# Performance work log

Measured on AMD Instinct MI355X. Metric: run time of the kernel, lower is better.

The kernel has to match this reference:

```python
import jax, jax.numpy as jnp
import numpy as np

D = 1024
H = 16
HD = D // H
SCALE = HD ** -0.5
EPS = 1e-5

def _ln(x, g, b):
    m = jnp.mean(x, axis=-1, keepdims=True)
    v = jnp.mean((x - m) ** 2, axis=-1, keepdims=True)
    return (x - m) / jnp.sqrt(v + EPS) * g + b

def setup_inputs() -> dict:
    key = jax.random.key(0)
    ks = jax.random.split(key, 16)
    B, Lq, Lk = 8, 1024, 1024
    s = 0.02
    inp = {
        "q": jax.random.normal(ks[0], (B, Lq, D), jnp.float32),
        "kv": jax.random.normal(ks[1], (B, Lk, D), jnp.float32),
        "kv_mask": jax.random.randint(ks[2], (B, Lk), 0, 2).astype(bool),
        "Wq": jax.random.normal(ks[3], (D, D), jnp.float32) * s,
        "bq": jnp.zeros((D,), jnp.float32),
        "Wk": jax.random.normal(ks[4], (D, D), jnp.float32) * s,
        "bk": jnp.zeros((D,), jnp.float32),
        "Wv": jax.random.normal(ks[5], (D, D), jnp.float32) * s,
        "bv": jnp.zeros((D,), jnp.float32),
        "Wo": jax.random.normal(ks[6], (D, D), jnp.float32) * s,
        "bo": jnp.zeros((D,), jnp.float32),
        "ln1_g": jnp.ones((D,), jnp.float32),
        "ln1_b": jnp.zeros((D,), jnp.float32),
        "W1": jax.random.normal(ks[7], (D, 4 * D), jnp.float32) * s,
        "b1": jnp.zeros((4 * D,), jnp.float32),
        "W2": jax.random.normal(ks[8], (4 * D, D), jnp.float32) * s,
        "b2": jnp.zeros((D,), jnp.float32),
        "ln2_g": jnp.ones((D,), jnp.float32),
        "ln2_b": jnp.zeros((D,), jnp.float32),
    }
    return inp

def reference(q, kv, kv_mask, Wq, bq, Wk, bk, Wv, bv, Wo, bo, ln1_g, ln1_b, W1, b1, W2, b2, ln2_g, ln2_b):
    B, Lq, _ = q.shape
    Lk = kv.shape[1]
    # projections -> [B, H, L, HD]
    qp = (q @ Wq + bq).reshape(B, Lq, H, HD).transpose(0, 2, 1, 3)
    kp = (kv @ Wk + bk).reshape(B, Lk, H, HD).transpose(0, 2, 1, 3)
    vp = (kv @ Wv + bv).reshape(B, Lk, H, HD).transpose(0, 2, 1, 3)
    scores = jnp.einsum('bhqd,bhkd->bhqk', qp, kp) * SCALE
    # mask: True = pad; if a row is all-pad, un-mask the last key position
    all_pad = jnp.all(kv_mask, axis=1)  # [B]
    mask = kv_mask.at[:, -1].set(jnp.where(all_pad, False, kv_mask[:, -1]))
    scores = jnp.where(mask[:, None, None, :], jnp.float32(-10000.0), scores)
    attn = jax.nn.softmax(scores, axis=-1)  # dropout is identity at eval
    out = jnp.einsum('bhqk,bhkd->bhqd', attn, vp)
    out = out.transpose(0, 2, 1, 3).reshape(B, Lq, D)
    out = out @ Wo + bo
    x = _ln(q + out, ln1_g, ln1_b)
    x2 = jax.nn.relu(x @ W1 + b1) @ W2 + b2
    return _ln(x + x2, ln2_g, ln2_b)
```

## Files before the change

kernel.cpp:

```cpp
#include <hip/hip_runtime.h>

typedef __bf16 bf16_t;
typedef bf16_t bf16x8 __attribute__((ext_vector_type(8)));
typedef bf16_t bf16x4 __attribute__((ext_vector_type(4)));
typedef float f32x4 __attribute__((ext_vector_type(4)));
typedef unsigned int u32;

typedef __attribute__((address_space(1))) unsigned as1_u32;
typedef __attribute__((address_space(3))) unsigned as3_u32;

#define LOG2E 1.4426950408889634f
#define QSCALE (0.125f * LOG2E)
#define MASK2 (-10000.0f * LOG2E)

__device__ __forceinline__ void gload16(const void* g, void* l) {
  __builtin_amdgcn_global_load_lds((as1_u32*)(void*)g, (as3_u32*)l, 16, 0, 0);
}

__global__ void cvt_qkv(const float* __restrict__ q, const float* __restrict__ kv,
                        bf16_t* __restrict__ qb, bf16_t* __restrict__ kvb) {
  long i = ((long)blockIdx.x * 256 + threadIdx.x) * 8;
  const float* src; bf16_t* dst;
  if (i < 8388608) { src = q + i; dst = qb + i; }
  else { src = kv + (i - 8388608); dst = kvb + (i - 8388608); }
  const float4 a = *(const float4*)src;
  const float4 b = *(const float4*)(src + 4);
  bf16x8 o;
  o[0] = (bf16_t)a.x; o[1] = (bf16_t)a.y; o[2] = (bf16_t)a.z; o[3] = (bf16_t)a.w;
  o[4] = (bf16_t)b.x; o[5] = (bf16_t)b.y; o[6] = (bf16_t)b.z; o[7] = (bf16_t)b.w;
  *(bf16x8*)dst = o;
}

__global__ void prep_mask(const unsigned char* __restrict__ mraw,
                          float* __restrict__ maskf) {
  __shared__ int sred[256];
  const int t = threadIdx.x, b = blockIdx.x;
  int f = 0;
  for (int i = t; i < 2048; i += 256) {
    u32 v = ((const u32*)mraw)[i];
    if (v & 0xFFFFFF00u) f = 1;
  }
  sred[t] = f; __syncthreads();
  for (int s = 128; s; s >>= 1) { if (t < s) sred[t] |= sred[t + s]; __syncthreads(); }
  const int isByte = sred[0];
  __syncthreads();

  int vals[4]; int allpad = 1;
#pragma unroll
  for (int i = 0; i < 4; i++) {
    int k = t * 4 + i;
    int mv = isByte ? (int)mraw[b * 1024 + k] : ((const int*)mraw)[b * 1024 + k];
    vals[i] = (mv != 0);
    allpad &= vals[i];
  }
  sred[t] = allpad; __syncthreads();
  for (int s = 128; s; s >>= 1) { if (t < s) sred[t] &= sred[t + s]; __syncthreads(); }
  const int ap = sred[0];
#pragma unroll
  for (int i = 0; i < 4; i++) {
    int k = t * 4 + i;
    int m = vals[i];
    if (ap && k == 1023) m = 0;
    maskf[b * 1024 + k] = m ? MASK2 : 0.0f;
  }
}

struct TP { const float* s; bf16_t* d; int K; int N; };
struct TP6 { TP t[6]; };
__global__ void transpose_all(TP6 args) {
  __shared__ float tile[64][65];
  int bid = blockIdx.x, z, tx, ty;
  if (bid < 1024)      { z = bid >> 8;  int r = bid & 255;  tx = r & 15; ty = r >> 4; }
  else if (bid < 2048) { z = 4;         int r = bid - 1024; tx = r & 63; ty = r >> 6; }
  else                 { z = 5;         int r = bid - 2048; tx = r & 15; ty = r >> 4; }
  const TP a = args.t[z];
  const int t = threadIdx.x;
  const int n0 = tx * 64, k0 = ty * 64;
#pragma unroll
  for (int i = 0; i < 16; i++) {
    int e = i * 256 + t; int r = e >> 6, c = e & 63;
    tile[r][c] = a.s[(size_t)(k0 + r) * a.N + n0 + c];
  }
  __syncthreads();
#pragma unroll
  for (int i = 0; i < 16; i++) {
    int e = i * 256 + t; int r = e >> 6, c = e & 63;
    a.d[(size_t)(n0 + r) * a.K + k0 + c] = (bf16_t)tile[c][r];
  }
}

template<int BM, int BN, int NT>
__global__ __launch_bounds__(NT, 2)
void gemm_bt(const bf16_t* __restrict__ A, const bf16_t* __restrict__ BT,
             const float* __restrict__ bias, bf16_t* __restrict__ C,
             int M, int N, int K, int relu, int bias_mode, float scale) {
  constexpr int WAVES = NT / 64;
  constexpr int WNC = (BN == 256) ? 4 : 2;
  constexpr int WMC = WAVES / WNC;
  constexpr int M_REP = BM / (WMC * 16);
  constexpr int N_REP = BN / (WNC * 16);
  constexpr int JA = BM * 8 / NT;
  constexpr int JB = BN * 8 / NT;

  __shared__ __align__(16) bf16_t As[2][BM * 64];
  __shared__ __align__(16) bf16_t Bs[2][BN * 64];

  const int tid = threadIdx.x;
  const int wave = tid >> 6, lane = tid & 63;
  const int quad = lane >> 4, l15 = lane & 15;
  const int gx = gridDim.x;
  const int nwg = gx * gridDim.y;
  int lin = blockIdx.y * gx + blockIdx.x;
  lin = (lin & 7) * (nwg >> 3) + (lin >> 3);
  const long bm = (long)(lin / gx) * BM, bn = (long)(lin % gx) * BN;
  const int wm = (wave / WNC) * (M_REP * 16), wn = (wave % WNC) * (N_REP * 16);

  const bf16_t* agp[JA];
  const bf16_t* bgp[JB];
#pragma unroll
  for (int j = 0; j < JA; j++) {
    int e = j * NT + tid, r = e >> 3, c = (e & 7) ^ (r & 7);
    agp[j] = A + (bm + r) * (long)K + c * 8;
  }
#pragma unroll
  for (int j = 0; j < JB; j++) {
    int e = j * NT + tid, r = e >> 3, c = (e & 7) ^ (r & 7);
    bgp[j] = BT + (bn + r) * (long)K + c * 8;
  }

  int aoff[M_REP][2], boff[N_REP][2];
#pragma unroll
  for (int mi = 0; mi < M_REP; mi++)
#pragma unroll
    for (int ks = 0; ks < 2; ks++) {
      int row = wm + mi * 16 + l15;
      aoff[mi][ks] = row * 64 + (((ks * 4 + quad) ^ (row & 7)) * 8);
    }
#pragma unroll
  for (int ni = 0; ni < N_REP; ni++)
#pragma unroll
    for (int ks = 0; ks < 2; ks++) {
      int row = wn + ni * 16 + l15;
      boff[ni][ks] = row * 64 + (((ks * 4 + quad) ^ (row & 7)) * 8);
    }

  f32x4 acc[M_REP][N_REP];
#pragma unroll
  for (int i = 0; i < M_REP; i++)
#pragma unroll
    for (int j = 0; j < N_REP; j++) acc[i][j] = (f32x4){0.f, 0.f, 0.f, 0.f};

  auto stage = [&](int kt, int s) {
#pragma unroll
    for (int j = 0; j < JA; j++)
      gload16(agp[j] + (long)kt * 64, &As[s][(j * NT + wave * 64) * 8]);
#pragma unroll
    for (int j = 0; j < JB; j++)
      gload16(bgp[j] + (long)kt * 64, &Bs[s][(j * NT + wave * 64) * 8]);
  };

  const int T = K >> 6;
  stage(0, 0);
  for (int t = 0; t < T; t++) {
    const int s = t & 1;
    if (t + 1 < T) {
      stage(t + 1, s ^ 1);
      asm volatile("s_waitcnt vmcnt(8)" ::: "memory");
    } else {
      asm volatile("s_waitcnt vmcnt(0)" ::: "memory");
    }
    __builtin_amdgcn_s_barrier();

#pragma unroll
    for (int ks = 0; ks < 2; ks++) {
      bf16x8 af[M_REP], bf[N_REP];
#pragma unroll
      for (int mi = 0; mi < M_REP; mi++) af[mi] = *(const bf16x8*)&As[s][aoff[mi][ks]];
#pragma unroll
      for (int ni = 0; ni < N_REP; ni++) bf[ni] = *(const bf16x8*)&Bs[s][boff[ni][ks]];
      __builtin_amdgcn_s_setprio(1);
#pragma unroll
      for (int mi = 0; mi < M_REP; mi++)
#pragma unroll
        for (int ni = 0; ni < N_REP; ni++)
          acc[mi][ni] = __builtin_amdgcn_mfma_f32_16x16x32_bf16(af[mi], bf[ni], acc[mi][ni], 0, 0, 0);
      __builtin_amdgcn_s_setprio(0);
    }
    asm volatile("s_waitcnt lgkmcnt(0)" ::: "memory");
    __builtin_amdgcn_s_barrier();
  }

#pragma unroll
  for (int mi = 0; mi < M_REP; mi++) {
#pragma unroll
    for (int ni = 0; ni < N_REP; ni++) {
      const long col = bn + wn + ni * 16 + l15;
      const float bc = bias_mode ? 0.f : bias[col];
#pragma unroll
      for (int r = 0; r < 4; r++) {
        const long row = bm + wm + mi * 16 + quad * 4 + r;
        const float bb = bias_mode ? bias[row] : bc;
        float v = (acc[mi][ni][r] + bb) * scale;
        if (relu) v = v > 0.f ? v : 0.f;
        C[row * N + col] = (bf16_t)v;
      }
    }
  }
}

__global__ __launch_bounds__(512, 2)
void gemm_8p(const bf16_t* __restrict__ A, const bf16_t* __restrict__ BT,
             const float* __restrict__ bias, bf16_t* __restrict__ C,
             int M, int N, int K, int relu, float scale) {
  __shared__ __align__(16) bf16_t As[2][256 * 64];
  __shared__ __align__(16) bf16_t Bs[2][256 * 64];

  const int tid = threadIdx.x;
  const int wave = tid >> 6, lane = tid & 63;
  const int quad = lane >> 4, l15 = lane & 15;
  const int g = wave >> 2;
  const int wn = (wave & 3) * 64;
  const int gx = gridDim.x;
  const int nwg = gx * gridDim.y;
  int lin = blockIdx.y * gx + blockIdx.x;
  lin = (lin & 7) * (nwg >> 3) + (lin >> 3);
  const long bm = (long)(lin / gx) * 256, bn = (long)(lin % gx) * 256;

  const int r_ = tid >> 3;
  const int cs_ = ((tid & 7) ^ (r_ & 7)) * 8;
  const int arow = r_ + ((r_ >= 32) ? 96 : 0);
  const bf16_t* ag = A + (bm + arow) * (long)K + cs_;
  const bf16_t* bg = BT + (bn + r_) * (long)K + cs_;

  int aoff[4][2][2], boff[4][2];
#pragma unroll
  for (int p = 0; p < 4; p++)
#pragma unroll
    for (int i = 0; i < 2; i++)
#pragma unroll
      for (int ks = 0; ks < 2; ks++) {
        int slot = p * 64 + g * 32 + i * 16 + l15;
        aoff[p][i][ks] = slot * 64 + (((ks * 4 + quad) ^ (l15 & 7)) * 8);
      }
#pragma unroll
  for (int ni = 0; ni < 4; ni++)
#pragma unroll
    for (int ks = 0; ks < 2; ks++) {
      int row = wn + ni * 16 + l15;
      boff[ni][ks] = row * 64 + (((ks * 4 + quad) ^ (row & 7)) * 8);
    }

  f32x4 acc[8][4];
#pragma unroll
  for (int i = 0; i < 8; i++)
#pragma unroll
    for (int j = 0; j < 4; j++) acc[i][j] = (f32x4){0.f, 0.f, 0.f, 0.f};

  auto stageB = [&](int kt, int s, int j) {
    gload16(bg + (long)(j * 64) * K + (long)kt * 64, &Bs[s][(j * 512 + wave * 64) * 8]);
  };
  auto stageA = [&](int kt, int s, int p) {
    gload16(ag + (long)(p * 32) * K + (long)kt * 64, &As[s][(p * 512 + wave * 64) * 8]);
  };

  const int T = K >> 6;
#pragma unroll
  for (int j = 0; j < 4; j++) stageB(0, 0, j);
#pragma unroll
  for (int p = 0; p < 4; p++) stageA(0, 0, p);

#pragma unroll 1
  for (int t = 0; t < T; t++) {
    const int s = t & 1;
    const bool pf = (t + 1 < T);

    bf16x8 bf[4][2];
#pragma unroll
    for (int p = 0; p < 4; p++) {
      if (p == 0)      { asm volatile("s_waitcnt vmcnt(3)" ::: "memory"); }
      else if (p == 1) { if (pf) asm volatile("s_waitcnt vmcnt(4)" ::: "memory");
                         else    asm volatile("s_waitcnt vmcnt(2)" ::: "memory"); }
      else if (p == 2) { if (pf) asm volatile("s_waitcnt vmcnt(5)" ::: "memory");
                         else    asm volatile("s_waitcnt vmcnt(1)" ::: "memory"); }
      else             { if (pf) asm volatile("s_waitcnt vmcnt(6)" ::: "memory");
                         else    asm volatile("s_waitcnt vmcnt(0)" ::: "memory"); }
      __builtin_amdgcn_s_barrier();

      if (p == 0) {
#pragma unroll
        for (int ni = 0; ni < 4; ni++)
#pragma unroll
          for (int ks = 0; ks < 2; ks++)
            bf[ni][ks] = *(const bf16x8*)&Bs[s][boff[ni][ks]];
      }
      bf16x8 af[2][2];
#pragma unroll
      for (int i = 0; i < 2; i++)
#pragma unroll
        for (int ks = 0; ks < 2; ks++)
          af[i][ks] = *(const bf16x8*)&As[s][aoff[p][i][ks]];

      if (pf) {
        if (p == 0)      { stageB(t + 1, s ^ 1, 0); stageB(t + 1, s ^ 1, 1); }
        else if (p == 1) { stageB(t + 1, s ^ 1, 2); stageB(t + 1, s ^ 1, 3); }
        else if (p == 2) { stageA(t + 1, s ^ 1, 0); stageA(t + 1, s ^ 1, 1); }
        else             { stageA(t + 1, s ^ 1, 2); stageA(t + 1, s ^ 1, 3); }
      }

      __builtin_amdgcn_s_setprio(1);
#pragma unroll
      for (int i = 0; i < 2; i++)
#pragma unroll
        for (int ni = 0; ni < 4; ni++)
#pragma unroll
          for (int ks = 0; ks < 2; ks++)
            acc[p * 2 + i][ni] = __builtin_amdgcn_mfma_f32_16x16x32_bf16(
                af[i][ks], bf[ni][ks], acc[p * 2 + i][ni], 0, 0, 0);
      __builtin_amdgcn_s_setprio(0);
    }
  }

#pragma unroll
  for (int mi = 0; mi < 8; mi++) {
#pragma unroll
    for (int ni = 0; ni < 4; ni++) {
      const long col = bn + wn + ni * 16 + l15;
      const float bc = bias[col];
#pragma unroll
      for (int r = 0; r < 4; r++) {
        const long row = bm + g * 128 + mi * 16 + quad * 4 + r;
        float v = (acc[mi][ni][r] + bc) * scale;
        if (relu) v = v > 0.f ? v : 0.f;
        C[row * N + col] = (bf16_t)v;
      }
    }
  }
}

__global__ __launch_bounds__(256, 4)
void attn(const bf16_t* __restrict__ Q, const bf16_t* __restrict__ Kp,
          const bf16_t* __restrict__ Vt, const float* __restrict__ maskf,
          bf16_t* __restrict__ AO) {
  __shared__ __align__(16) bf16_t Qs[64 * 64];
  __shared__ __align__(16) bf16_t Ks[64 * 64];
  __shared__ __align__(16) bf16_t Vts[64 * 64];
  __shared__ __align__(16) bf16_t Ps[4][16 * 64];
  __shared__ __align__(16) float msk[64];

  const int tid = threadIdx.x;
  const int wave = tid >> 6, lane = tid & 63;
  const int quad = lane >> 4, l15 = lane & 15;
  int lin = (blockIdx.z * 16 + blockIdx.y) * 16 + blockIdx.x;
  lin = (lin & 7) * 256 + (lin >> 3);
  const int q0 = (lin & 15) * 64;
  const int h = (lin >> 4) & 15;
  const int b = lin >> 8;

  const long base_q = ((long)b * 1024 + q0) * 1024 + h * 64;
  const long base_k = (long)b * 1024 * 1024 + h * 64;
  const long base_v = (long)h * 64 * 8192 + b * 1024;

  const int r0 = tid >> 3;
  const int c0 = ((tid & 7) ^ (r0 & 7)) * 8;
  const int r1 = (256 + tid) >> 3;
  const int c1 = (((256 + tid) & 7) ^ (r1 & 7)) * 8;
  const int wd0 = wave * 64 * 8;
  const int wd1 = (256 + wave * 64) * 8;

  const bf16_t* qg0 = Q + base_q + (long)r0 * 1024 + c0;
  const bf16_t* qg1 = Q + base_q + (long)r1 * 1024 + c1;
  const bf16_t* kg0 = Kp + base_k + (long)r0 * 1024 + c0;
  const bf16_t* kg1 = Kp + base_k + (long)r1 * 1024 + c1;
  const bf16_t* vg0 = Vt + base_v + (long)r0 * 8192 + c0;
  const bf16_t* vg1 = Vt + base_v + (long)r1 * 8192 + c1;
  const float* mrow = maskf + b * 1024;

  gload16(qg0, &Qs[wd0]);
  gload16(qg1, &Qs[wd1]);

  int offKV[4][2], offP[2], pwOff[4];
#pragma unroll
  for (int nt = 0; nt < 4; nt++)
#pragma unroll
    for (int ks = 0; ks < 2; ks++)
      offKV[nt][ks] = (nt * 16 + l15) * 64 + (((ks * 4 + quad) ^ (l15 & 7)) * 8);
#pragma unroll
  for (int ks = 0; ks < 2; ks++)
    offP[ks] = l15 * 64 + (((ks * 4 + quad) ^ (l15 & 7)) * 8);
#pragma unroll
  for (int nt = 0; nt < 4; nt++)
    pwOff[nt] = l15 * 64 + (((nt * 2 + (quad >> 1)) ^ (l15 & 7)) * 8) + (quad & 1) * 4;

  __syncthreads();

  bf16x8 aq[2];
#pragma unroll
  for (int ks = 0; ks < 2; ks++) {
    const int row = wave * 16 + l15;
    aq[ks] = *(const bf16x8*)&Qs[row * 64 + (((ks * 4 + quad) ^ (row & 7)) * 8)];
  }

  float l_i = 0.f;
  f32x4 o[4];
#pragma unroll
  for (int nt = 0; nt < 4; nt++) o[nt] = (f32x4){0.f, 0.f, 0.f, 0.f};

  bf16_t* Pw = &Ps[wave][0];

  for (int kt = 0; kt < 16; kt++) {
    const int k0 = kt * 64;
    __syncthreads();
    gload16(kg0 + (long)k0 * 1024, &Ks[wd0]);
    gload16(kg1 + (long)k0 * 1024, &Ks[wd1]);
    gload16(vg0 + k0, &Vts[wd0]);
    gload16(vg1 + k0, &Vts[wd1]);
    if (tid < 64) msk[tid] = mrow[k0 + tid];
    __syncthreads();

    f32x4 mv[4];
#pragma unroll
    for (int nt = 0; nt < 4; nt++)
      mv[nt] = *(const f32x4*)&msk[nt * 16 + quad * 4];

    f32x4 sc[4];
#pragma unroll
    for (int nt = 0; nt < 4; nt++) {
      f32x4 s = mv[nt];
#pragma unroll
      for (int ks = 0; ks < 2; ks++) {
        bf16x8 bk = *(const bf16x8*)&Ks[offKV[nt][ks]];
        s = __builtin_amdgcn_mfma_f32_16x16x32_bf16(bk, aq[ks], s, 0, 0, 0);
      }
      sc[nt] = s;
    }

#pragma unroll
    for (int nt = 0; nt < 4; nt++)
#pragma unroll
      for (int r = 0; r < 4; r++) {
        const float p = exp2f(sc[nt][r]);
        sc[nt][r] = p;
        l_i += p;
      }

#pragma unroll
    for (int nt = 0; nt < 4; nt++) {
      bf16x4 pv;
#pragma unroll
      for (int r = 0; r < 4; r++) pv[r] = (bf16_t)sc[nt][r];
      *(bf16x4*)&Pw[pwOff[nt]] = pv;
    }

#pragma unroll
    for (int ks = 0; ks < 2; ks++) {
      bf16x8 ap = *(const bf16x8*)&Pw[offP[ks]];
#pragma unroll
      for (int nt = 0; nt < 4; nt++) {
        bf16x8 bv = *(const bf16x8*)&Vts[offKV[nt][ks]];
        o[nt] = __builtin_amdgcn_mfma_f32_16x16x32_bf16(ap, bv, o[nt], 0, 0, 0);
      }
    }
  }

  l_i += __shfl_xor(l_i, 16);
  l_i += __shfl_xor(l_i, 32);
  float linv[4];
#pragma unroll
  for (int r = 0; r < 4; r++)
    linv[r] = 1.0f / __shfl(l_i, (quad << 4) | (quad * 4 + r));
#pragma unroll
  for (int r = 0; r < 4; r++) {
    const int row = q0 + wave * 16 + quad * 4 + r;
#pragma unroll
    for (int nt = 0; nt < 4; nt++) {
      const int col = h * 64 + nt * 16 + l15;
      AO[((long)b * 1024 + row) * 1024 + col] = (bf16_t)(o[nt][r] * linv[r]);
    }
  }
}

__global__ __launch_bounds__(256)
void ln_res1(const float* __restrict__ xa, const bf16_t* __restrict__ xb,
             const float* __restrict__ g, const float* __restrict__ bt,
             bf16_t* __restrict__ out) {
  __shared__ float sw[8];
  const int t = threadIdx.x, w = t >> 6;
  const long row = blockIdx.x;
  const float4 a = *(const float4*)(xa + row * 1024 + t * 4);
  const bf16x4 bq = *(const bf16x4*)(xb + row * 1024 + t * 4);
  float v[4] = {a.x + (float)bq[0], a.y + (float)bq[1],
                a.z + (float)bq[2], a.w + (float)bq[3]};
  float s = v[0] + v[1] + v[2] + v[3];
  float s2 = v[0]*v[0] + v[1]*v[1] + v[2]*v[2] + v[3]*v[3];
#pragma unroll
  for (int off = 1; off < 64; off <<= 1) {
    s += __shfl_xor(s, off); s2 += __shfl_xor(s2, off);
  }
  if ((t & 63) == 0) { sw[w] = s; sw[4 + w] = s2; }
  __syncthreads();
  s = sw[0] + sw[1] + sw[2] + sw[3];
  s2 = sw[4] + sw[5] + sw[6] + sw[7];
  const float mean = s * (1.f / 1024.f);
  const float var = s2 * (1.f / 1024.f) - mean * mean;
  const float rstd = rsqrtf(var + 1e-5f);
  bf16x4 o;
#pragma unroll
  for (int i = 0; i < 4; i++) {
    const int c = t * 4 + i;
    o[i] = (bf16_t)((v[i] - mean) * rstd * g[c] + bt[c]);
  }
  *(bf16x4*)(out + row * 1024 + t * 4) = o;
}

__global__ __launch_bounds__(256)
void ln_res2(const bf16_t* __restrict__ xa, const bf16_t* __restrict__ xb,
             const float* __restrict__ g, const float* __restrict__ bt,
             float* __restrict__ out) {
  __shared__ float sw[8];
  const int t = threadIdx.x, w = t >> 6;
  const long row = blockIdx.x;
  const bf16x4 aq = *(const bf16x4*)(xa + row * 1024 + t * 4);
  const bf16x4 bq = *(const bf16x4*)(xb + row * 1024 + t * 4);
  float v[4];
#pragma unroll
  for (int i = 0; i < 4; i++) v[i] = (float)aq[i] + (float)bq[i];
  float s = v[0] + v[1] + v[2] + v[3];
  float s2 = v[0]*v[0] + v[1]*v[1] + v[2]*v[2] + v[3]*v[3];
#pragma unroll
  for (int off = 1; off < 64; off <<= 1) {
    s += __shfl_xor(s, off); s2 += __shfl_xor(s2, off);
  }
  if ((t & 63) == 0) { sw[w] = s; sw[4 + w] = s2; }
  __syncthreads();
  s = sw[0] + sw[1] + sw[2] + sw[3];
  s2 = sw[4] + sw[5] + sw[6] + sw[7];
  const float mean = s * (1.f / 1024.f);
  const float var = s2 * (1.f / 1024.f) - mean * mean;
  const float rstd = rsqrtf(var + 1e-5f);
  float4 o;
  o.x = (v[0] - mean) * rstd * g[t*4+0] + bt[t*4+0];
  o.y = (v[1] - mean) * rstd * g[t*4+1] + bt[t*4+1];
  o.z = (v[2] - mean) * rstd * g[t*4+2] + bt[t*4+2];
  o.w = (v[3] - mean) * rstd * g[t*4+3] + bt[t*4+3];
  *(float4*)(out + row * 1024 + t * 4) = o;
}

extern "C" void kernel_launch(void* const* d_in, const int* in_sizes, int n_in,
                              void* d_out, int out_size, void* d_ws, size_t ws_size,
                              hipStream_t stream) {
  (void)in_sizes; (void)n_in; (void)out_size; (void)ws_size;
  const float* q   = (const float*)d_in[0];
  const float* kv  = (const float*)d_in[1];
  const unsigned char* mraw = (const unsigned char*)d_in[2];
  const float* Wq = (const float*)d_in[3];
  const float* bq = (const float*)d_in[4];
  const float* Wk = (const float*)d_in[5];
  const float* bk = (const float*)d_in[6];
  const float* Wv = (const float*)d_in[7];
  const float* bv = (const float*)d_in[8];
  const float* Wo = (const float*)d_in[9];
  const float* bo = (const float*)d_in[10];
  const float* g1 = (const float*)d_in[11];
  const float* be1 = (const float*)d_in[12];
  const float* W1 = (const float*)d_in[13];
  const float* b1 = (const float*)d_in[14];
  const float* W2 = (const float*)d_in[15];
  const float* b2 = (const float*)d_in[16];
  const float* g2 = (const float*)d_in[17];
  const float* be2 = (const float*)d_in[18];
  float* out = (float*)d_out;

  char* ws = (char*)d_ws;
  size_t off = 0;
  auto alloc = [&](size_t bytes) -> char* {
    char* p = ws + off; off += (bytes + 255) & ~(size_t)255; return p;
  };
  const size_t MB16 = (size_t)8192 * 1024 * 2;
  float*  maskf = (float*)alloc(8192 * 4);
  bf16_t* WqT = (bf16_t*)alloc((size_t)1024 * 1024 * 2);
  bf16_t* WkT = (bf16_t*)alloc((size_t)1024 * 1024 * 2);
  bf16_t* WvT = (bf16_t*)alloc((size_t)1024 * 1024 * 2);
  bf16_t* WoT = (bf16_t*)alloc((size_t)1024 * 1024 * 2);
  bf16_t* W1T = (bf16_t*)alloc((size_t)1024 * 4096 * 2);
  bf16_t* W2T = (bf16_t*)alloc((size_t)4096 * 1024 * 2);
  bf16_t* Qp = (bf16_t*)alloc(MB16);
  bf16_t* Kp = (bf16_t*)alloc(MB16);
  bf16_t* VT = (bf16_t*)alloc(MB16);
  bf16_t* AO = (bf16_t*)alloc(MB16);
  bf16_t* X1 = (bf16_t*)alloc(MB16);
  bf16_t* TL = (bf16_t*)alloc(MB16);
  bf16_t* qb  = X1;
  bf16_t* kvb = TL;
  bf16_t* HF  = Qp;
  bf16_t* OP  = Kp;
  bf16_t* F2  = WqT;

  cvt_qkv<<<8192, 256, 0, stream>>>(q, kv, qb, kvb);
  prep_mask<<<8, 256, 0, stream>>>(mraw, maskf);
  TP6 tp = {{ {Wq, WqT, 1024, 1024}, {Wk, WkT, 1024, 1024},
              {Wv, WvT, 1024, 1024}, {Wo, WoT, 1024, 1024},
              {W1, W1T, 1024, 4096}, {W2, W2T, 4096, 1024} }};
  transpose_all<<<3072, 256, 0, stream>>>(tp);

  const dim3 gproj(8, 64);
  gemm_bt<128,128,256><<<gproj, 256, 0, stream>>>(qb,  WqT, bq, Qp, 8192, 1024, 1024, 0, 0, QSCALE);
  gemm_bt<128,128,256><<<gproj, 256, 0, stream>>>(kvb, WkT, bk, Kp, 8192, 1024, 1024, 0, 0, 1.f);
  gemm_bt<128,128,256><<<dim3(64, 8), 256, 0, stream>>>(WvT, kvb, bv, VT, 1024, 8192, 1024, 0, 1, 1.f);

  attn<<<dim3(16, 16, 8), 256, 0, stream>>>(Qp, Kp, VT, maskf, AO);

  gemm_bt<128,128,256><<<gproj, 256, 0, stream>>>(AO, WoT, bo, OP, 8192, 1024, 1024, 0, 0, 1.f);
  ln_res1<<<8192, 256, 0, stream>>>(q, OP, g1, be1, X1);

  gemm_8p<<<dim3(16, 32), 512, 0, stream>>>(X1, W1T, b1, HF, 8192, 4096, 1024, 1, 1.f);
  gemm_bt<128,128,256><<<gproj, 256, 0, stream>>>(HF, W2T, b2, F2, 8192, 1024, 4096, 0, 0, 1.f);
  ln_res2<<<8192, 256, 0, stream>>>(X1, F2, g2, be2, out);
}
```

Baseline: 514.0 us.

## Replace 128x128 GEMMs with templated 8-wave 256xBN phased-pipeline GEMM

Removes the simple double-buffered 128x128 gemm_bt kernel and generalizes the 8-wave, 4-phase interleaved-prefetch gemm_8p kernel over BN (128 or 256), adding bias_mode support. All projection, output and FFN2 GEMMs now use 256x128 tiles with 512 threads, and prefetch is spread across phases with adjusted vmcnt waits. The intent is more reuse per tile and better overlap of loads with MFMA. In exchange there are fewer workgroups (256 per GEMM) on a many-CU device, and the handwritten wait counts are more fragile.

```diff
diff --git a/kernel.cpp b/kernel.cpp
--- a/kernel.cpp
+++ b/kernel.cpp
@@ -89,142 +89,26 @@
   }
 }
 
-template<int BM, int BN, int NT>
-__global__ __launch_bounds__(NT, 2)
-void gemm_bt(const bf16_t* __restrict__ A, const bf16_t* __restrict__ BT,
+template<int BN>
+__global__ __launch_bounds__(512, 2)
+void gemm_8p(const bf16_t* __restrict__ A, const bf16_t* __restrict__ BT,
              const float* __restrict__ bias, bf16_t* __restrict__ C,
              int M, int N, int K, int relu, int bias_mode, float scale) {
-  constexpr int WAVES = NT / 64;
-  constexpr int WNC = (BN == 256) ? 4 : 2;
-  constexpr int WMC = WAVES / WNC;
-  constexpr int M_REP = BM / (WMC * 16);
-  constexpr int N_REP = BN / (WNC * 16);
-  constexpr int JA = BM * 8 / NT;
-  constexpr int JB = BN * 8 / NT;
-
-  __shared__ __align__(16) bf16_t As[2][BM * 64];
+  constexpr int JB = BN * 8 / 512;
+  constexpr int N_REP = BN / 64;
+  __shared__ __align__(16) bf16_t As[2][256 * 64];
   __shared__ __align__(16) bf16_t Bs[2][BN * 64];
 
   const int tid = threadIdx.x;
   const int wave = tid >> 6, lane = tid & 63;
   const int quad = lane >> 4, l15 = lane & 15;
+  const int g = wave >> 2;
+  const int wn = (wave & 3) * (N_REP * 16);
   const int gx = gridDim.x;
   const int nwg = gx * gridDim.y;
   int lin = blockIdx.y * gx + blockIdx.x;
   lin = (lin & 7) * (nwg >> 3) + (lin >> 3);
-  const long bm = (long)(lin / gx) * BM, bn = (long)(lin % gx) * BN;
-  const int wm = (wave / WNC) * (M_REP * 16), wn = (wave % WNC) * (N_REP * 16);
-
-  const bf16_t* agp[JA];
-  const bf16_t* bgp[JB];
-#pragma unroll
-  for (int j = 0; j < JA; j++) {
-    int e = j * NT + tid, r = e >> 3, c = (e & 7) ^ (r & 7);
-    agp[j] = A + (bm + r) * (long)K + c * 8;
-  }
-#pragma unroll
-  for (int j = 0; j < JB; j++) {
-    int e = j * NT + tid, r = e >> 3, c = (e & 7) ^ (r & 7);
-    bgp[j] = BT + (bn + r) * (long)K + c * 8;
-  }
-
-  int aoff[M_REP][2], boff[N_REP][2];
-#pragma unroll
-  for (int mi = 0; mi < M_REP; mi++)
-#pragma unroll
-    for (int ks = 0; ks < 2; ks++) {
-      int row = wm + mi * 16 + l15;
-      aoff[mi][ks] = row * 64 + (((ks * 4 + quad) ^ (row & 7)) * 8);
-    }
-#pragma unroll
-  for (int ni = 0; ni < N_REP; ni++)
-#pragma unroll
-    for (int ks = 0; ks < 2; ks++) {
-      int row = wn + ni * 16 + l15;
-      boff[ni][ks] = row * 64 + (((ks * 4 + quad) ^ (row & 7)) * 8);
-    }
-
-  f32x4 acc[M_REP][N_REP];
-#pragma unroll
-  for (int i = 0; i < M_REP; i++)
-#pragma unroll
-    for (int j = 0; j < N_REP; j++) acc[i][j] = (f32x4){0.f, 0.f, 0.f, 0.f};
-
-  auto stage = [&](int kt, int s) {
-#pragma unroll
-    for (int j = 0; j < JA; j++)
-      gload16(agp[j] + (long)kt * 64, &As[s][(j * NT + wave * 64) * 8]);
-#pragma unroll
-    for (int j = 0; j < JB; j++)
-      gload16(bgp[j] + (long)kt * 64, &Bs[s][(j * NT + wave * 64) * 8]);
-  };
-
-  const int T = K >> 6;
-  stage(0, 0);
-  for (int t = 0; t < T; t++) {
-    const int s = t & 1;
-    if (t + 1 < T) {
-      stage(t + 1, s ^ 1);
-      asm volatile("s_waitcnt vmcnt(8)" ::: "memory");
-    } else {
-      asm volatile("s_waitcnt vmcnt(0)" ::: "memory");
-    }
-    __builtin_amdgcn_s_barrier();
-
-#pragma unroll
-    for (int ks = 0; ks < 2; ks++) {
-      bf16x8 af[M_REP], bf[N_REP];
-#pragma unroll
-      for (int mi = 0; mi < M_REP; mi++) af[mi] = *(const bf16x8*)&As[s][aoff[mi][ks]];
-#pragma unroll
-      for (int ni = 0; ni < N_REP; ni++) bf[ni] = *(const bf16x8*)&Bs[s][boff[ni][ks]];
-      __builtin_amdgcn_s_setprio(1);
-#pragma unroll
-      for (int mi = 0; mi < M_REP; mi++)
-#pragma unroll
-        for (int ni = 0; ni < N_REP; ni++)
-          acc[mi][ni] = __builtin_amdgcn_mfma_f32_16x16x32_bf16(af[mi], bf[ni], acc[mi][ni], 0, 0, 0);
-      __builtin_amdgcn_s_setprio(0);
-    }
-    asm volatile("s_waitcnt lgkmcnt(0)" ::: "memory");
-    __builtin_amdgcn_s_barrier();
-  }
-
-#pragma unroll
-  for (int mi = 0; mi < M_REP; mi++) {
-#pragma unroll
-    for (int ni = 0; ni < N_REP; ni++) {
-      const long col = bn + wn + ni * 16 + l15;
-      const float bc = bias_mode ? 0.f : bias[col];
-#pragma unroll
-      for (int r = 0; r < 4; r++) {
-        const long row = bm + wm + mi * 16 + quad * 4 + r;
-        const float bb = bias_mode ? bias[row] : bc;
-        float v = (acc[mi][ni][r] + bb) * scale;
-        if (relu) v = v > 0.f ? v : 0.f;
-        C[row * N + col] = (bf16_t)v;
-      }
-    }
-  }
-}
-
-__global__ __launch_bounds__(512, 2)
-void gemm_8p(const bf16_t* __restrict__ A, const bf16_t* __restrict__ BT,
-             const float* __restrict__ bias, bf16_t* __restrict__ C,
-             int M, int N, int K, int relu, float scale) {
-  __shared__ __align__(16) bf16_t As[2][256 * 64];
-  __shared__ __align__(16) bf16_t Bs[2][256 * 64];
-
-  const int tid = threadIdx.x;
-  const int wave = tid >> 6, lane = tid & 63;
-  const int quad = lane >> 4, l15 = lane & 15;
-  const int g = wave >> 2;
-  const int wn = (wave & 3) * 64;
-  const int gx = gridDim.x;
-  const int nwg = gx * gridDim.y;
-  int lin = blockIdx.y * gx + blockIdx.x;
-  lin = (lin & 7) * (nwg >> 3) + (lin >> 3);
-  const long bm = (long)(lin / gx) * 256, bn = (long)(lin % gx) * 256;
+  const long bm = (long)(lin / gx) * 256, bn = (long)(lin % gx) * BN;
 
   const int r_ = tid >> 3;
   const int cs_ = ((tid & 7) ^ (r_ & 7)) * 8;
@@ -232,7 +116,7 @@
   const bf16_t* ag = A + (bm + arow) * (long)K + cs_;
   const bf16_t* bg = BT + (bn + r_) * (long)K + cs_;
 
-  int aoff[4][2][2], boff[4][2];
+  int aoff[4][2][2], boff[N_REP][2];
 #pragma unroll
   for (int p = 0; p < 4; p++)
 #pragma unroll
@@ -243,18 +127,18 @@
         aoff[p][i][ks] = slot * 64 + (((ks * 4 + quad) ^ (l15 & 7)) * 8);
       }
 #pragma unroll
-  for (int ni = 0; ni < 4; ni++)
+  for (int ni = 0; ni < N_REP; ni++)
 #pragma unroll
     for (int ks = 0; ks < 2; ks++) {
       int row = wn + ni * 16 + l15;
       boff[ni][ks] = row * 64 + (((ks * 4 + quad) ^ (row & 7)) * 8);
     }
 
-  f32x4 acc[8][4];
+  f32x4 acc[8][N_REP];
 #pragma unroll
   for (int i = 0; i < 8; i++)
 #pragma unroll
-    for (int j = 0; j < 4; j++) acc[i][j] = (f32x4){0.f, 0.f, 0.f, 0.f};
+    for (int j = 0; j < N_REP; j++) acc[i][j] = (f32x4){0.f, 0.f, 0.f, 0.f};
 
   auto stageB = [&](int kt, int s, int j) {
     gload16(bg + (long)(j * 64) * K + (long)kt * 64, &Bs[s][(j * 512 + wave * 64) * 8]);
@@ -265,7 +149,7 @@
 
   const int T = K >> 6;
 #pragma unroll
-  for (int j = 0; j < 4; j++) stageB(0, 0, j);
+  for (int j = 0; j < JB; j++) stageB(0, 0, j);
 #pragma unroll
   for (int p = 0; p < 4; p++) stageA(0, 0, p);
 
@@ -274,21 +158,31 @@
     const int s = t & 1;
     const bool pf = (t + 1 < T);
 
-    bf16x8 bf[4][2];
+    bf16x8 bf[N_REP][2];
 #pragma unroll
     for (int p = 0; p < 4; p++) {
-      if (p == 0)      { asm volatile("s_waitcnt vmcnt(3)" ::: "memory"); }
-      else if (p == 1) { if (pf) asm volatile("s_waitcnt vmcnt(4)" ::: "memory");
-                         else    asm volatile("s_waitcnt vmcnt(2)" ::: "memory"); }
-      else if (p == 2) { if (pf) asm volatile("s_waitcnt vmcnt(5)" ::: "memory");
-                         else    asm volatile("s_waitcnt vmcnt(1)" ::: "memory"); }
-      else             { if (pf) asm volatile("s_waitcnt vmcnt(6)" ::: "memory");
-                         else    asm volatile("s_waitcnt vmcnt(0)" ::: "memory"); }
+      if constexpr (JB == 4) {
+        if (p == 0)      { asm volatile("s_waitcnt vmcnt(3)" ::: "memory"); }
+        else if (p == 1) { if (pf) asm volatile("s_waitcnt vmcnt(4)" ::: "memory");
+                           else    asm volatile("s_waitcnt vmcnt(2)" ::: "memory"); }
+        else if (p == 2) { if (pf) asm volatile("s_waitcnt vmcnt(5)" ::: "memory");
+                           else    asm volatile("s_waitcnt vmcnt(1)" ::: "memory"); }
+        else             { if (pf) asm volatile("s_waitcnt vmcnt(6)" ::: "memory");
+                           else    asm volatile("s_waitcnt vmcnt(0)" ::: "memory"); }
+      } else {
+        if (p == 0)      { asm volatile("s_waitcnt vmcnt(3)" ::: "memory"); }
+        else if (p == 1) { if (pf) asm volatile("s_waitcnt vmcnt(3)" ::: "memory");
+                           else    asm volatile("s_waitcnt vmcnt(2)" ::: "memory"); }
+        else if (p == 2) { if (pf) asm volatile("s_waitcnt vmcnt(3)" ::: "memory");
+                           else    asm volatile("s_waitcnt vmcnt(1)" ::: "memory"); }
+        else             { if (pf) asm volatile("s_waitcnt vmcnt(4)" ::: "memory");
+                           else    asm volatile("s_waitcnt vmcnt(0)" ::: "memory"); }
+      }
       __builtin_amdgcn_s_barrier();
 
       if (p == 0) {
 #pragma unroll
-        for (int ni = 0; ni < 4; ni++)
+        for (int ni = 0; ni < N_REP; ni++)
 #pragma unroll
           for (int ks = 0; ks < 2; ks++)
             bf[ni][ks] = *(const bf16x8*)&Bs[s][boff[ni][ks]];
@@ -301,17 +195,24 @@
           af[i][ks] = *(const bf16x8*)&As[s][aoff[p][i][ks]];
 
       if (pf) {
-        if (p == 0)      { stageB(t + 1, s ^ 1, 0); stageB(t + 1, s ^ 1, 1); }
-        else if (p == 1) { stageB(t + 1, s ^ 1, 2); stageB(t + 1, s ^ 1, 3); }
-        else if (p == 2) { stageA(t + 1, s ^ 1, 0); stageA(t + 1, s ^ 1, 1); }
-        else             { stageA(t + 1, s ^ 1, 2); stageA(t + 1, s ^ 1, 3); }
+        if constexpr (JB == 4) {
+          if (p == 0)      { stageB(t + 1, s ^ 1, 0); stageB(t + 1, s ^ 1, 1); }
+          else if (p == 1) { stageB(t + 1, s ^ 1, 2); stageB(t + 1, s ^ 1, 3); }
+          else if (p == 2) { stageA(t + 1, s ^ 1, 0); stageA(t + 1, s ^ 1, 1); }
+          else             { stageA(t + 1, s ^ 1, 2); stageA(t + 1, s ^ 1, 3); }
+        } else {
+          if (p == 0)      { stageB(t + 1, s ^ 1, 0); }
+          else if (p == 1) { stageB(t + 1, s ^ 1, 1); }
+          else if (p == 2) { stageA(t + 1, s ^ 1, 0); stageA(t + 1, s ^ 1, 1); }
+          else             { stageA(t + 1, s ^ 1, 2); stageA(t + 1, s ^ 1, 3); }
+        }
       }
 
       __builtin_amdgcn_s_setprio(1);
 #pragma unroll
       for (int i = 0; i < 2; i++)
 #pragma unroll
-        for (int ni = 0; ni < 4; ni++)
+        for (int ni = 0; ni < N_REP; ni++)
 #pragma unroll
           for (int ks = 0; ks < 2; ks++)
             acc[p * 2 + i][ni] = __builtin_amdgcn_mfma_f32_16x16x32_bf16(
@@ -323,13 +224,14 @@
 #pragma unroll
   for (int mi = 0; mi < 8; mi++) {
 #pragma unroll
-    for (int ni = 0; ni < 4; ni++) {
+    for (int ni = 0; ni < N_REP; ni++) {
       const long col = bn + wn + ni * 16 + l15;
-      const float bc = bias[col];
+      const float bc = bias_mode ? 0.f : bias[col];
 #pragma unroll
       for (int r = 0; r < 4; r++) {
         const long row = bm + g * 128 + mi * 16 + quad * 4 + r;
-        float v = (acc[mi][ni][r] + bc) * scale;
+        const float bb = bias_mode ? bias[row] : bc;
+        float v = (acc[mi][ni][r] + bb) * scale;
         if (relu) v = v > 0.f ? v : 0.f;
         C[row * N + col] = (bf16_t)v;
       }
@@ -602,17 +504,16 @@
               {W1, W1T, 1024, 4096}, {W2, W2T, 4096, 1024} }};
   transpose_all<<<3072, 256, 0, stream>>>(tp);
 
-  const dim3 gproj(8, 64);
-  gemm_bt<128,128,256><<<gproj, 256, 0, stream>>>(qb,  WqT, bq, Qp, 8192, 1024, 1024, 0, 0, QSCALE);
-  gemm_bt<128,128,256><<<gproj, 256, 0, stream>>>(kvb, WkT, bk, Kp, 8192, 1024, 1024, 0, 0, 1.f);
-  gemm_bt<128,128,256><<<dim3(64, 8), 256, 0, stream>>>(WvT, kvb, bv, VT, 1024, 8192, 1024, 0, 1, 1.f);
+  gemm_8p<128><<<dim3(8, 32), 512, 0, stream>>>(qb,  WqT, bq, Qp, 8192, 1024, 1024, 0, 0, QSCALE);
+  gemm_8p<128><<<dim3(8, 32), 512, 0, stream>>>(kvb, WkT, bk, Kp, 8192, 1024, 1024, 0, 0, 1.f);
+  gemm_8p<128><<<dim3(64, 4), 512, 0, stream>>>(WvT, kvb, bv, VT, 1024, 8192, 1024, 0, 1, 1.f);
 
   attn<<<dim3(16, 16, 8), 256, 0, stream>>>(Qp, Kp, VT, maskf, AO);
 
-  gemm_bt<128,128,256><<<gproj, 256, 0, stream>>>(AO, WoT, bo, OP, 8192, 1024, 1024, 0, 0, 1.f);
+  gemm_8p<128><<<dim3(8, 32), 512, 0, stream>>>(AO, WoT, bo, OP, 8192, 1024, 1024, 0, 0, 1.f);
   ln_res1<<<8192, 256, 0, stream>>>(q, OP, g1, be1, X1);
 
-  gemm_8p<<<dim3(16, 32), 512, 0, stream>>>(X1, W1T, b1, HF, 8192, 4096, 1024, 1, 1.f);
-  gemm_bt<128,128,256><<<gproj, 256, 0, stream>>>(HF, W2T, b2, F2, 8192, 1024, 4096, 0, 0, 1.f);
+  gemm_8p<256><<<dim3(16, 32), 512, 0, stream>>>(X1, W1T, b1, HF, 8192, 4096, 1024, 1, 0, 1.f);
+  gemm_8p<128><<<dim3(8, 32), 512, 0, stream>>>(HF, W2T, b2, F2, 8192, 1024, 4096, 0, 0, 1.f);
   ln_res2<<<8192, 256, 0, stream>>>(X1, F2, g2, be2, out);
 }
```

Result: slower. 553.7 us (+7.7%).
